# Kernel tuning notes

Measured on AMD Instinct MI355X. Metric: run time of the kernel, lower is better.

Reference implementation:

```python
import jax, jax.numpy as jnp
import numpy as np
import math

D_MODEL = 1024
N_HEAD = 16


def setup_inputs() -> dict:
    key = jax.random.key(0)
    ks = jax.random.split(key, 5)
    x = jax.random.normal(ks[0], (2, 2048, D_MODEL), dtype=jnp.float32)
    # Linear params (torch Linear: y = x @ W.T + b); store as [in, out] for einsum
    s1 = 1.0 / math.sqrt(D_MODEL)
    W_qkv = jax.random.uniform(ks[1], (D_MODEL, 3 * D_MODEL), jnp.float32, -s1, s1)
    b_qkv = jax.random.uniform(ks[2], (3 * D_MODEL,), jnp.float32, -s1, s1)
    W_out = jax.random.uniform(ks[3], (D_MODEL, D_MODEL), jnp.float32, -s1, s1)
    b_out = jax.random.uniform(ks[4], (D_MODEL,), jnp.float32, -s1, s1)
    return {"x": x, "W_qkv": W_qkv, "b_qkv": b_qkv, "W_out": W_out, "b_out": b_out}


def reference(x, W_qkv, b_qkv, W_out, b_out):
    B, L, D = x.shape
    H = N_HEAD
    hd = D // H
    qkv = x @ W_qkv + b_qkv                      # [B, L, 3D]
    q, k, v = jnp.split(qkv, 3, axis=-1)
    # [B, H, L, hd]
    q = q.reshape(B, L, H, hd).transpose(0, 2, 1, 3)
    k = k.reshape(B, L, H, hd).transpose(0, 2, 1, 3)
    v = v.reshape(B, L, H, hd).transpose(0, 2, 1, 3)
    scale = 1.0 / math.sqrt(hd)
    scores = jnp.einsum('bhqd,bhkd->bhqk', q, k) * scale   # [B, H, L, L]
    causal = jnp.tril(jnp.ones((L, L), dtype=bool))
    scores = jnp.where(causal, scores, jnp.float32(-jnp.inf))
    probs = jax.nn.softmax(scores, axis=-1)
    out = jnp.einsum('bhqk,bhkd->bhqd', probs, v)          # [B, H, L, hd]
    out = out.transpose(0, 2, 1, 3).reshape(B, L, D)
    out = out @ W_out + b_out
    return jnp.squeeze(out)
```

## Files before the change

kernel.cpp:

```cpp
#include <hip/hip_runtime.h>
#include <hip/hip_bf16.h>

#define SEQ    2048
#define NHEAD  16
#define HD     64
#define DMODEL 1024

using bf16 = __hip_bfloat16;
using short8 = __attribute__((ext_vector_type(8))) short;
using short4v = __attribute__((ext_vector_type(4))) short;
using f32x4  = __attribute__((ext_vector_type(4))) float;

__device__ __forceinline__ float fast_exp2(float x) {
  return __builtin_amdgcn_exp2f(x);
}
#define WAIT_LGKM0() __builtin_amdgcn_s_waitcnt(0xC07F)

__device__ __forceinline__ void gload_lds16(const bf16* g, bf16* l) {
  __builtin_amdgcn_global_load_lds(
      (const __attribute__((address_space(1))) void*)g,
      (__attribute__((address_space(3))) void*)l, 16, 0, 0);
}


__global__ void prep_k(const float* __restrict__ x, bf16* __restrict__ xb,
                       const float* __restrict__ Wqkv, bf16* __restrict__ WqkvT,
                       const float* __restrict__ Wout, bf16* __restrict__ WoutT) {
  __shared__ bf16 tile[32][33];
  const int id = blockIdx.x, tid = threadIdx.x;
  if (id < 2048) {
    int i = (id * 256 + tid) * 8;
    bf16 tmp[8];
    #pragma unroll
    for (int j = 0; j < 8; ++j) tmp[j] = __float2bfloat16(x[i + j]);
    *(short8*)&xb[i] = *(short8*)tmp;
    return;
  }
  const float* in; bf16* out; int R, C, tx32, ty32;
  if (id < 2048 + 3072) {
    int t = id - 2048; in = Wqkv; out = WqkvT; R = 1024; C = 3072;
    tx32 = t % 96; ty32 = t / 96;
  } else {
    int t = id - 5120; in = Wout; out = WoutT; R = 1024; C = 1024;
    tx32 = t % 32; ty32 = t / 32;
  }
  int c0 = tx32 * 32, r0 = ty32 * 32;
  int tx = tid & 31, ty = tid >> 5;
  #pragma unroll
  for (int i = ty; i < 32; i += 8)
    tile[i][tx] = __float2bfloat16(in[(size_t)(r0 + i) * C + c0 + tx]);
  __syncthreads();
  #pragma unroll
  for (int i = ty; i < 32; i += 8)
    out[(size_t)(c0 + i) * R + r0 + tx] = tile[tx][i];
}

__global__ void transpose_v_k(const bf16* __restrict__ in, bf16* __restrict__ out) {
  __shared__ bf16 tile[32][33];
  const int bh = blockIdx.z;
  const bf16* ip = in  + (size_t)bh * SEQ * HD;
  bf16* op       = out + (size_t)bh * HD * SEQ;
  int c0 = blockIdx.x * 32, r0 = blockIdx.y * 32;
  int tx = threadIdx.x & 31, ty = threadIdx.x >> 5;
  #pragma unroll
  for (int i = ty; i < 32; i += 8)
    tile[i][tx] = ip[(size_t)(r0 + i) * HD + c0 + tx];
  __syncthreads();
  #pragma unroll
  for (int i = ty; i < 32; i += 8)
    op[(size_t)(c0 + i) * SEQ + r0 + tx] = tile[tx][i];
}

template <int MODE>
__global__ __launch_bounds__(256)
void gemm_bt(const bf16* __restrict__ A, const bf16* __restrict__ BT,
             const float* __restrict__ bias,
             bf16* __restrict__ out0, bf16* __restrict__ out1,
             bf16* __restrict__ out2, float* __restrict__ outf) {
  constexpr int K = 1024;
  __shared__ __align__(16) bf16 As[128 * 32];
  __shared__ __align__(16) bf16 Bs[128 * 32];
  const int tid = threadIdx.x;
  const int wave = tid >> 6, lane = tid & 63;
  const int quad = lane >> 4, l16 = lane & 15;
  const int waveM = (wave >> 1) * 64, waveN = (wave & 1) * 64;
  const int m0 = blockIdx.x * 128, n0 = blockIdx.y * 128;
  const int srow = (lane >> 2);
  const int scol = (((lane & 3) ^ ((lane >> 3) & 3)) * 8);
  const int q8   = (quad ^ ((l16 >> 1) & 3)) * 8;

  const f32x4 zero4 = {0.f, 0.f, 0.f, 0.f};
  f32x4 acc[4][4];
  #pragma unroll
  for (int i = 0; i < 4; ++i)
    #pragma unroll
    for (int j = 0; j < 4; ++j) acc[i][j] = zero4;

  for (int k0 = 0; k0 < K; k0 += 32) {
    __syncthreads();
    #pragma unroll
    for (int half = 0; half < 2; ++half) {
      int grow = half * 64 + wave * 16 + srow;
      gload_lds16(&A [(size_t)(m0 + grow) * K + k0 + scol],
                  &As[(half * 64 + wave * 16) * 32]);
      gload_lds16(&BT[(size_t)(n0 + grow) * K + k0 + scol],
                  &Bs[(half * 64 + wave * 16) * 32]);
    }
    __syncthreads();
    short8 af[4], bfm[4];
    #pragma unroll
    for (int mt = 0; mt < 4; ++mt)
      af[mt] = *(const short8*)&As[(waveM + mt * 16 + l16) * 32 + q8];
    #pragma unroll
    for (int nt = 0; nt < 4; ++nt)
      bfm[nt] = *(const short8*)&Bs[(waveN + nt * 16 + l16) * 32 + q8];
    #pragma unroll
    for (int mt = 0; mt < 4; ++mt)
      #pragma unroll
      for (int nt = 0; nt < 4; ++nt)
        acc[mt][nt] = __builtin_amdgcn_mfma_f32_16x16x32_bf16(
            af[mt], bfm[nt], acc[mt][nt], 0, 0, 0);
  }

  #pragma unroll
  for (int nt = 0; nt < 4; ++nt) {
    int n = n0 + waveN + nt * 16 + l16;
    float bvv = bias[n];
    #pragma unroll
    for (int mt = 0; mt < 4; ++mt) {
      #pragma unroll
      for (int r = 0; r < 4; ++r) {
        int m = m0 + waveM + mt * 16 + quad * 4 + r;
        float v = acc[mt][nt][r] + bvv;
        if (MODE == 1) {
          outf[(size_t)m * 1024 + n] = v;
        } else {
          bf16 v16 = __float2bfloat16(v);
          int which = n >> 10, oo = n & 1023;
          int h = oo >> 6, c = oo & 63;
          int b = m >> 11, l = m & 2047;
          size_t idx = ((size_t)(b * NHEAD + h) * SEQ + l) * HD + c;
          if (which == 0)      out0[idx] = v16;
          else if (which == 1) out1[idx] = v16;
          else                 out2[idx] = v16;
        }
      }
    }
  }
}

__global__ __launch_bounds__(256)
void attn_k(const bf16* __restrict__ Q, const bf16* __restrict__ Kb,
            const bf16* __restrict__ VT, bf16* __restrict__ O) {
  __shared__ __align__(16) bf16 Ks[2][128 * 32];
  __shared__ __align__(16) bf16 Vs[4][64 * 32];
  __shared__ __align__(16) bf16 Plds[4][16][136];
  const int tid = threadIdx.x;
  const int wave = tid >> 6, lane = tid & 63;
  const int quad = lane >> 4, l16 = lane & 15;
  const int srow = lane >> 2;
  const int scol = (((lane & 3) ^ ((lane >> 3) & 3)) * 8);
  const int q8   = (quad ^ ((l16 >> 1) & 3)) * 8;
  const int id = blockIdx.x;
  const int bh = id & 31, blkx = id >> 5;
  const int b = bh >> 4, h = bh & 15;

  const bf16* Qp = Q  + (size_t)bh * SEQ * HD;
  const bf16* Kp = Kb + (size_t)bh * SEQ * HD;
  const bf16* Vp = VT + (size_t)bh * HD * SEQ;

  const f32x4 zero4 = {0.f, 0.f, 0.f, 0.f};
  const float c = 0.18033688011112042f;
  const float mc = 8.0f * c;

  for (int pass = 0; pass < 2; ++pass) {
    const int qt = pass ? (15 - blkx) : blkx;
    const int q0w = qt * 128 + wave * 32;
    const int ntiles = qt + 1;

    short8 qf[2][2];
    #pragma unroll
    for (int qg = 0; qg < 2; ++qg) {
      qf[qg][0] = *(const short8*)&Qp[(size_t)(q0w + qg * 16 + l16) * HD + quad * 8];
      qf[qg][1] = *(const short8*)&Qp[(size_t)(q0w + qg * 16 + l16) * HD + 32 + quad * 8];
    }

    f32x4 oacc[2][4];
    #pragma unroll
    for (int qg = 0; qg < 2; ++qg)
      #pragma unroll
      for (int dt = 0; dt < 4; ++dt) oacc[qg][dt] = zero4;
    float l4[2][4] = {{0.f,0.f,0.f,0.f},{0.f,0.f,0.f,0.f}};

    for (int t = 0; t < ntiles; ++t) {
      const int k0 = t << 7;
      __syncthreads();
      #pragma unroll
      for (int i = 0; i < 2; ++i)
        #pragma unroll
        for (int hh = 0; hh < 2; ++hh)
          gload_lds16(&Kp[(size_t)(k0 + wave * 32 + i * 16 + srow) * HD + hh * 32 + scol],
                      &Ks[hh][(wave * 32 + i * 16) * 32]);
      #pragma unroll
      for (int g = 0; g < 4; ++g)
        gload_lds16(&Vp[(size_t)(g * 16 + srow) * SEQ + k0 + wave * 32 + scol],
                    &Vs[wave][(g * 16) * 32]);
      __syncthreads();

      f32x4 s0[8], s1[8];
      #pragma unroll
      for (int g = 0; g < 8; ++g) {
        short8 ka = *(const short8*)&Ks[0][(g * 16 + l16) * 32 + q8];
        short8 kb = *(const short8*)&Ks[1][(g * 16 + l16) * 32 + q8];
        f32x4 a = zero4, bb = zero4;
        a  = __builtin_amdgcn_mfma_f32_16x16x32_bf16(ka, qf[0][0], a, 0, 0, 0);
        a  = __builtin_amdgcn_mfma_f32_16x16x32_bf16(kb, qf[0][1], a, 0, 0, 0);
        bb = __builtin_amdgcn_mfma_f32_16x16x32_bf16(ka, qf[1][0], bb, 0, 0, 0);
        bb = __builtin_amdgcn_mfma_f32_16x16x32_bf16(kb, qf[1][1], bb, 0, 0, 0);
        s0[g] = a; s1[g] = bb;
      }

      if (t == ntiles - 1) {
        #pragma unroll
        for (int g = 0; g < 8; ++g)
          #pragma unroll
          for (int r = 0; r < 4; ++r) {
            int k = k0 + g * 16 + quad * 4 + r;
            s0[g][r] = (k <= q0w + l16)      ? s0[g][r] : -__builtin_inff();
            s1[g][r] = (k <= q0w + 16 + l16) ? s1[g][r] : -__builtin_inff();
          }
      }

      #pragma unroll
      for (int qg = 0; qg < 2; ++qg) {
        f32x4* s = qg ? s1 : s0;
        #pragma unroll
        for (int g = 0; g < 8; ++g) {
          bf16 pb[4];
          #pragma unroll
          for (int r = 0; r < 4; ++r) {
            float p = fast_exp2(__builtin_fmaf(s[g][r], c, -mc));
            l4[qg][r] += p;
            pb[r] = __float2bfloat16(p);
          }
          *(short4v*)&Plds[wave][l16][g * 16 + quad * 4] = *(short4v*)pb;
        }
        WAIT_LGKM0();
        #pragma unroll
        for (int ch = 0; ch < 4; ++ch) {
          short8 pf = *(const short8*)&Plds[wave][l16][ch * 32 + quad * 8];
          #pragma unroll
          for (int dt = 0; dt < 4; ++dt) {
            short8 vf = *(const short8*)&Vs[ch][(dt * 16 + l16) * 32 + q8];
            oacc[qg][dt] = __builtin_amdgcn_mfma_f32_16x16x32_bf16(
                vf, pf, oacc[qg][dt], 0, 0, 0);
          }
        }
      }
    }

    #pragma unroll
    for (int qg = 0; qg < 2; ++qg) {
      float l_i = (l4[qg][0] + l4[qg][1]) + (l4[qg][2] + l4[qg][3]);
      l_i += __shfl_xor(l_i, 16, 64);
      l_i += __shfl_xor(l_i, 32, 64);
      float inv = 1.f / l_i;
      #pragma unroll
      for (int dt = 0; dt < 4; ++dt) {
        bf16 ob[4];
        #pragma unroll
        for (int r = 0; r < 4; ++r) ob[r] = __float2bfloat16(oacc[qg][dt][r] * inv);
        *(short4v*)&Plds[wave][l16][dt * 16 + quad * 4] = *(short4v*)ob;
      }
      WAIT_LGKM0();
      int row = lane >> 2;
      int col = (lane & 3) * 16;
      short8 o0 = *(const short8*)&Plds[wave][row][col];
      short8 o1 = *(const short8*)&Plds[wave][row][col + 8];
      size_t base = ((size_t)(b * SEQ + q0w + qg * 16 + row)) * DMODEL + h * HD + col;
      *(short8*)&O[base]     = o0;
      *(short8*)&O[base + 8] = o1;
      WAIT_LGKM0();
    }
  }
}

extern "C" void kernel_launch(void* const* d_in, const int* in_sizes, int n_in,
                              void* d_out, int out_size, void* d_ws, size_t ws_size,
                              hipStream_t stream) {
  const float* x    = (const float*)d_in[0];
  const float* Wqkv = (const float*)d_in[1];
  const float* bqkv = (const float*)d_in[2];
  const float* Wout = (const float*)d_in[3];
  const float* bout = (const float*)d_in[4];
  float* out = (float*)d_out;

  char* ws = (char*)d_ws;
  const size_t MB = 1024 * 1024;
  char* big    = ws + 16384;
  bf16* Kbuf   = (bf16*)(big);
  bf16* VTb    = (bf16*)(big + 8 * MB);
  bf16* xb     = (bf16*)(big + 16 * MB);
  bf16* AO     = (bf16*)(big + 16 * MB);
  bf16* WqkvT  = (bf16*)(big + 24 * MB);
  bf16* WoutT  = (bf16*)(big + 30 * MB);
  bf16* Qb     = (bf16*)d_out;
  bf16* Vtmp   = (bf16*)((char*)d_out + 8 * MB);

  prep_k<<<6144, 256, 0, stream>>>(x, xb, Wqkv, WqkvT, Wout, WoutT);
  gemm_bt<0><<<dim3(4096 / 128, 3072 / 128), 256, 0, stream>>>(
      xb, WqkvT, bqkv, Qb, Kbuf, Vtmp, nullptr);
  transpose_v_k<<<dim3(HD / 32, SEQ / 32, 32), 256, 0, stream>>>(Vtmp, VTb);
  attn_k<<<256, 256, 0, stream>>>(Qb, Kbuf, VTb, AO);
  gemm_bt<1><<<dim3(4096 / 128, 1024 / 128), 256, 0, stream>>>(
      AO, WoutT, bout, nullptr, nullptr, nullptr, out);
}
```

Before: 192.4 us.

## Halve attention query tile to 64 rows and double block count

The attention kernel now gives each block 64 query rows (16 per wave) instead of 128 (32 per wave) and launches 512 blocks instead of 256. The paired causal pass now spans 32 query tiles while keeping 128-wide key tiles. This is meant to fill more CUs on MI355X and cut per-wave register pressure, since only one set of score and output accumulators is kept. In exchange, each K/V tile loaded into LDS is reused by half as many query rows, so total K/V traffic and barrier overhead double, and diagonal tiles waste more masked work.

Measured after the change: 181.1 us. 1.06x faster.

```diff
diff --git a/kernel.cpp b/kernel.cpp
--- a/kernel.cpp
+++ b/kernel.cpp
@@ -174,23 +174,18 @@
   const float mc = 8.0f * c;
 
   for (int pass = 0; pass < 2; ++pass) {
-    const int qt = pass ? (15 - blkx) : blkx;
-    const int q0w = qt * 128 + wave * 32;
-    const int ntiles = qt + 1;
-
-    short8 qf[2][2];
-    #pragma unroll
-    for (int qg = 0; qg < 2; ++qg) {
-      qf[qg][0] = *(const short8*)&Qp[(size_t)(q0w + qg * 16 + l16) * HD + quad * 8];
-      qf[qg][1] = *(const short8*)&Qp[(size_t)(q0w + qg * 16 + l16) * HD + 32 + quad * 8];
-    }
-
-    f32x4 oacc[2][4];
-    #pragma unroll
-    for (int qg = 0; qg < 2; ++qg)
-      #pragma unroll
-      for (int dt = 0; dt < 4; ++dt) oacc[qg][dt] = zero4;
-    float l4[2][4] = {{0.f,0.f,0.f,0.f},{0.f,0.f,0.f,0.f}};
+    const int qt = pass ? (31 - blkx) : blkx;
+    const int q0w = qt * 64 + wave * 16;
+    const int q_lane = q0w + l16;
+    const int ntiles = (qt + 2) >> 1;
+
+    short8 qf0 = *(const short8*)&Qp[(size_t)(q0w + l16) * HD + quad * 8];
+    short8 qf1 = *(const short8*)&Qp[(size_t)(q0w + l16) * HD + 32 + quad * 8];
+
+    f32x4 oacc[4];
+    #pragma unroll
+    for (int dt = 0; dt < 4; ++dt) oacc[dt] = zero4;
+    float l4[4] = {0.f, 0.f, 0.f, 0.f};
 
     for (int t = 0; t < ntiles; ++t) {
       const int k0 = t << 7;
@@ -207,17 +202,15 @@
                     &Vs[wave][(g * 16) * 32]);
       __syncthreads();
 
-      f32x4 s0[8], s1[8];
+      f32x4 s[8];
       #pragma unroll
       for (int g = 0; g < 8; ++g) {
         short8 ka = *(const short8*)&Ks[0][(g * 16 + l16) * 32 + q8];
         short8 kb = *(const short8*)&Ks[1][(g * 16 + l16) * 32 + q8];
-        f32x4 a = zero4, bb = zero4;
-        a  = __builtin_amdgcn_mfma_f32_16x16x32_bf16(ka, qf[0][0], a, 0, 0, 0);
-        a  = __builtin_amdgcn_mfma_f32_16x16x32_bf16(kb, qf[0][1], a, 0, 0, 0);
-        bb = __builtin_amdgcn_mfma_f32_16x16x32_bf16(ka, qf[1][0], bb, 0, 0, 0);
-        bb = __builtin_amdgcn_mfma_f32_16x16x32_bf16(kb, qf[1][1], bb, 0, 0, 0);
-        s0[g] = a; s1[g] = bb;
+        f32x4 sg = zero4;
+        sg = __builtin_amdgcn_mfma_f32_16x16x32_bf16(ka, qf0, sg, 0, 0, 0);
+        sg = __builtin_amdgcn_mfma_f32_16x16x32_bf16(kb, qf1, sg, 0, 0, 0);
+        s[g] = sg;
       }
 
       if (t == ntiles - 1) {
@@ -226,62 +219,59 @@
           #pragma unroll
           for (int r = 0; r < 4; ++r) {
             int k = k0 + g * 16 + quad * 4 + r;
-            s0[g][r] = (k <= q0w + l16)      ? s0[g][r] : -__builtin_inff();
-            s1[g][r] = (k <= q0w + 16 + l16) ? s1[g][r] : -__builtin_inff();
+            s[g][r] = (k <= q_lane) ? s[g][r] : -__builtin_inff();
           }
       }
 
       #pragma unroll
-      for (int qg = 0; qg < 2; ++qg) {
-        f32x4* s = qg ? s1 : s0;
+      for (int g = 0; g < 8; ++g) {
+        bf16 pb[4];
         #pragma unroll
-        for (int g = 0; g < 8; ++g) {
-          bf16 pb[4];
-          #pragma unroll
-          for (int r = 0; r < 4; ++r) {
-            float p = fast_exp2(__builtin_fmaf(s[g][r], c, -mc));
-            l4[qg][r] += p;
-            pb[r] = __float2bfloat16(p);
-          }
-          *(short4v*)&Plds[wave][l16][g * 16 + quad * 4] = *(short4v*)pb;
+        for (int r = 0; r < 4; ++r) {
+          float p = fast_exp2(__builtin_fmaf(s[g][r], c, -mc));
+          l4[r] += p;
+          pb[r] = __float2bfloat16(p);
         }
-        WAIT_LGKM0();
-        #pragma unroll
-        for (int ch = 0; ch < 4; ++ch) {
-          short8 pf = *(const short8*)&Plds[wave][l16][ch * 32 + quad * 8];
-          #pragma unroll
-          for (int dt = 0; dt < 4; ++dt) {
-            short8 vf = *(const short8*)&Vs[ch][(dt * 16 + l16) * 32 + q8];
-            oacc[qg][dt] = __builtin_amdgcn_mfma_f32_16x16x32_bf16(
-                vf, pf, oacc[qg][dt], 0, 0, 0);
-          }
-        }
-      }
-    }
-
-    #pragma unroll
-    for (int qg = 0; qg < 2; ++qg) {
-      float l_i = (l4[qg][0] + l4[qg][1]) + (l4[qg][2] + l4[qg][3]);
-      l_i += __shfl_xor(l_i, 16, 64);
-      l_i += __shfl_xor(l_i, 32, 64);
-      float inv = 1.f / l_i;
-      #pragma unroll
-      for (int dt = 0; dt < 4; ++dt) {
-        bf16 ob[4];
-        #pragma unroll
-        for (int r = 0; r < 4; ++r) ob[r] = __float2bfloat16(oacc[qg][dt][r] * inv);
-        *(short4v*)&Plds[wave][l16][dt * 16 + quad * 4] = *(short4v*)ob;
+        *(short4v*)&Plds[wave][l16][g * 16 + quad * 4] = *(short4v*)pb;
       }
       WAIT_LGKM0();
+
+      short8 pf[4];
+      #pragma unroll
+      for (int ch = 0; ch < 4; ++ch)
+        pf[ch] = *(const short8*)&Plds[wave][l16][ch * 32 + quad * 8];
+      #pragma unroll
+      for (int ch = 0; ch < 4; ++ch)
+        #pragma unroll
+        for (int dt = 0; dt < 4; ++dt) {
+          short8 vf = *(const short8*)&Vs[ch][(dt * 16 + l16) * 32 + q8];
+          oacc[dt] = __builtin_amdgcn_mfma_f32_16x16x32_bf16(vf, pf[ch], oacc[dt], 0, 0, 0);
+        }
+    }
+
+    float l_i = (l4[0] + l4[1]) + (l4[2] + l4[3]);
+    l_i += __shfl_xor(l_i, 16, 64);
+    l_i += __shfl_xor(l_i, 32, 64);
+    float inv = 1.f / l_i;
+
+    #pragma unroll
+    for (int dt = 0; dt < 4; ++dt) {
+      bf16 ob[4];
+      #pragma unroll
+      for (int r = 0; r < 4; ++r) ob[r] = __float2bfloat16(oacc[dt][r] * inv);
+      *(short4v*)&Plds[wave][l16][dt * 16 + quad * 4] = *(short4v*)ob;
+    }
+    WAIT_LGKM0();
+    {
       int row = lane >> 2;
       int col = (lane & 3) * 16;
       short8 o0 = *(const short8*)&Plds[wave][row][col];
       short8 o1 = *(const short8*)&Plds[wave][row][col + 8];
-      size_t base = ((size_t)(b * SEQ + q0w + qg * 16 + row)) * DMODEL + h * HD + col;
+      size_t base = ((size_t)(b * SEQ + q0w + row)) * DMODEL + h * HD + col;
       *(short8*)&O[base]     = o0;
       *(short8*)&O[base + 8] = o1;
-      WAIT_LGKM0();
-    }
+    }
+    WAIT_LGKM0();
   }
 }
 
@@ -311,7 +301,7 @@
   gemm_bt<0><<<dim3(4096 / 128, 3072 / 128), 256, 0, stream>>>(
       xb, WqkvT, bqkv, Qb, Kbuf, Vtmp, nullptr);
   transpose_v_k<<<dim3(HD / 32, SEQ / 32, 32), 256, 0, stream>>>(Vtmp, VTb);
-  attn_k<<<256, 256, 0, stream>>>(Qb, Kbuf, VTb, AO);
+  attn_k<<<512, 256, 0, stream>>>(Qb, Kbuf, VTb, AO);
   gemm_bt<1><<<dim3(4096 / 128, 1024 / 128), 256, 0, stream>>>(
       AO, WoutT, bout, nullptr, nullptr, nullptr, out);
 }
```
